# Optimization experiments

Measured on AMD Instinct MI355X. Metric: run time of the kernel, lower is better.

Reference implementation:

```python
import jax, jax.numpy as jnp
import numpy as np
import math

B, Hi, Wi, D = 4, 56, 56, 256
Ho, Wo = Hi // 2, Wi // 2
HEADS, HD = D // 32, 32
NUM_ITERS, DEPTH = 3, 2
KG, KB = 3, 7
LN_EPS = 1e-5

def _ln(x, g, b):
    m = x.mean(-1, keepdims=True)
    v = ((x - m) ** 2).mean(-1, keepdims=True)
    return (x - m) * jax.lax.rsqrt(v + LN_EPS) * g + b

def _na_idx(L, K):
    # NATten neighborhood: window clamped at borders, always K neighbors
    return jnp.clip(jnp.arange(L) - K // 2, 0, L - K)[:, None] + jnp.arange(K)[None, :]

def _gather_nb(t, K):  # t [B,n,H,W,D] -> [B,n,H,K,W,K,D]
    H, W = t.shape[2], t.shape[3]
    return t[:, :, _na_idx(H, K)][:, :, :, :, _na_idx(W, K)]

def _na2d_qk(query, key, K):  # query attends to K*K neighbors of key
    b, n, H, W, d = query.shape
    return jnp.einsum('bnijd,bniajcd->bnijac', query, _gather_nb(key, K)).reshape(b, n, H, W, K * K)

def _na2d_av(attn, v, K):
    b, n, H, W, _ = attn.shape
    return jnp.einsum('bnijac,bniajcd->bnijd', attn.reshape(b, n, H, W, K, K), _gather_nb(v, K))

def _rope_cos_sin(N, hd):
    f = 1.0 / (10000.0 ** (jnp.arange(0, hd, 2, dtype=jnp.float32) / hd))
    ang = jnp.arange(N, dtype=jnp.float32)[:, None] * f[None, :]
    return jnp.cos(ang), jnp.sin(ang)

def _apply_rope(x, cos, sin):  # x [B,N,h,hd], interleaved pairs
    x2 = x.reshape(x.shape[:-1] + (-1, 2))
    x0, x1 = x2[..., 0], x2[..., 1]
    c, s = cos[None, :, None, :], sin[None, :, None, :]
    return jnp.stack([x0 * c - x1 * s, x1 * c + x0 * s], -1).reshape(x.shape)

def _forward(x, g_seed_w, g_q_w, g_k_w, g_v_w, g_mlp_w1, g_mlp_b1, g_mlp_w2, g_mlp_b2,
             g_ln_in_g, g_ln_in_b, g_ln_out_g, g_ln_out_b, g_tau, g_rpb,
             blk_ln1_g, blk_ln1_b, blk_qkv_w, blk_proj_w, blk_proj_b,
             blk_ln2_g, blk_ln2_b, blk_mlp_w1, blk_mlp_b1, blk_mlp_w2, blk_mlp_b2):
    Bx = x.shape[0]
    ln_out = lambda t: _ln(t, g_ln_out_g, g_ln_out_b)

    def to_groups(t):  # [B,N_in,D] -> [B,4,Ho,Wo,D], group p = 2*ph+pw (F.unfold 2x2 s2 order)
        m = t.reshape(Bx, Ho, 2, Wo, 2, D).transpose(0, 2, 4, 1, 3, 5)
        return m.reshape(Bx, 4, Ho, Wo, D)

    # ---- SparseGroupingLayer (local) ----
    k = to_groups(_ln(x, g_ln_in_g, g_ln_in_b) @ g_k_w.T)
    v = to_groups(x @ g_v_w.T)
    seed = jax.lax.conv_general_dilated(
        x.reshape(Bx, Hi, Wi, D), g_seed_w.transpose(2, 3, 1, 0),
        (2, 2), ((1, 1), (1, 1)), dimension_numbers=('NHWC', 'HWIO', 'NHWC'))
    x_out = ln_out(seed.reshape(Bx, Ho * Wo, D))

    ih, iw = _na_idx(Ho, KG), _na_idx(Wo, KG)
    q_idx = (ih[:, None, :, None] * Wo + iw[None, :, None, :]).reshape(-1)  # [Ho*Wo*9]
    ids_full = jnp.tile(q_idx, 4)  # same idx map for all 4 groups
    rpb = g_rpb[None, :, None, None, :]
    scale_g = jnp.exp(g_tau[0])

    for _ in range(NUM_ITERS):
        q = (ln_out(x_out) @ g_q_w.T).reshape(Bx, 1, Ho, Wo, D)
        attn = _na2d_qk(k, jnp.broadcast_to(q, (Bx, 4, Ho, Wo, D)), KG) + rpb
        attn = jax.nn.softmax(attn * scale_g, axis=-1) + 1e-6  # [B,4,Ho,Wo,9]
        col = jnp.zeros((Bx, Ho * Wo), attn.dtype).at[:, ids_full].add(attn.reshape(Bx, -1))
        denom = col[:, ids_full].reshape(Bx, 4, Ho, Wo, KG * KG)
        A_col = attn / (denom + 1e-8)
        x_out = x_out + _na2d_av(A_col, v, KG).sum(axis=1).reshape(Bx, Ho * Wo, D)
        h = jax.nn.gelu(x_out @ g_mlp_w1.T + g_mlp_b1, approximate=False) @ g_mlp_w2.T + g_mlp_b2
        x_out = x_out + ln_out(h)

    # ---- SeNaTraBlocks (local neighborhood attention, window 7, RoPE) ----
    cos, sin = _rope_cos_sin(Ho * Wo, HD)
    sc = HD ** -0.5
    for l in range(DEPTH):
        h = _ln(x_out, blk_ln1_g[l], blk_ln1_b[l])
        qkv = (h @ blk_qkv_w[l].T).reshape(Bx, Ho * Wo, 3, HEADS, HD)
        q, kk, vv = qkv[:, :, 0], qkv[:, :, 1], qkv[:, :, 2]  # [B,N,h,hd]
        q = _apply_rope(q, cos, sin).transpose(0, 2, 1, 3).reshape(Bx, HEADS, Ho, Wo, HD)
        kk = _apply_rope(kk, cos, sin).transpose(0, 2, 1, 3).reshape(Bx, HEADS, Ho, Wo, HD)
        vv = vv.transpose(0, 2, 1, 3).reshape(Bx, HEADS, Ho, Wo, HD)
        a = jax.nn.softmax(_na2d_qk(q, kk, KB) * sc, axis=-1)
        o = _na2d_av(a, vv, KB).transpose(0, 2, 3, 1, 4).reshape(Bx, Ho * Wo, D)
        x_out = x_out + (o @ blk_proj_w[l].T + blk_proj_b[l])
        h2 = _ln(x_out, blk_ln2_g[l], blk_ln2_b[l])
        m = jax.nn.gelu(h2 @ blk_mlp_w1[l].T + blk_mlp_b1[l], approximate=False) @ blk_mlp_w2[l].T + blk_mlp_b2[l]
        x_out = x_out + m
    return x_out

def setup_inputs():
    key = jax.random.key(0)
    ks = jax.random.split(key, 16)
    w = lambda k, s: jax.random.normal(k, s, dtype=jnp.float32) * 0.02
    Hm = int(D * 3.0)
    return {
        'x': jax.random.normal(ks[0], (B, Hi * Wi, D), dtype=jnp.float32),
        'g_seed_w': w(ks[1], (D, D, 3, 3)),
        'g_q_w': w(ks[2], (D, D)), 'g_k_w': w(ks[3], (D, D)), 'g_v_w': w(ks[4], (D, D)),
        'g_mlp_w1': w(ks[5], (2 * D, D)), 'g_mlp_b1': jnp.zeros((2 * D,), jnp.float32),
        'g_mlp_w2': w(ks[6], (D, 2 * D)), 'g_mlp_b2': jnp.zeros((D,), jnp.float32),
        'g_ln_in_g': jnp.ones((D,), jnp.float32), 'g_ln_in_b': jnp.zeros((D,), jnp.float32),
        'g_ln_out_g': jnp.ones((D,), jnp.float32), 'g_ln_out_b': jnp.zeros((D,), jnp.float32),
        'g_tau': jnp.full((1,), math.log(D ** -0.5), jnp.float32),
        'g_rpb': w(ks[7], (4, 9)),
        'blk_ln1_g': jnp.ones((DEPTH, D), jnp.float32), 'blk_ln1_b': jnp.zeros((DEPTH, D), jnp.float32),
        'blk_qkv_w': w(ks[8], (DEPTH, 3 * D, D)),
        'blk_proj_w': w(ks[9], (DEPTH, D, D)), 'blk_proj_b': jnp.zeros((DEPTH, D), jnp.float32),
        'blk_ln2_g': jnp.ones((DEPTH, D), jnp.float32), 'blk_ln2_b': jnp.zeros((DEPTH, D), jnp.float32),
        'blk_mlp_w1': w(ks[10], (DEPTH, Hm, D)), 'blk_mlp_b1': jnp.zeros((DEPTH, Hm), jnp.float32),
        'blk_mlp_w2': w(ks[11], (DEPTH, D, Hm)), 'blk_mlp_b2': jnp.zeros((DEPTH, D), jnp.float32),
    }

def reference(x, g_seed_w, g_q_w, g_k_w, g_v_w, g_mlp_w1, g_mlp_b1, g_mlp_w2, g_mlp_b2,
              g_ln_in_g, g_ln_in_b, g_ln_out_g, g_ln_out_b, g_tau, g_rpb,
              blk_ln1_g, blk_ln1_b, blk_qkv_w, blk_proj_w, blk_proj_b,
              blk_ln2_g, blk_ln2_b, blk_mlp_w1, blk_mlp_b1, blk_mlp_w2, blk_mlp_b2):
    return _forward(x, g_seed_w, g_q_w, g_k_w, g_v_w, g_mlp_w1, g_mlp_b1, g_mlp_w2, g_mlp_b2,
                    g_ln_in_g, g_ln_in_b, g_ln_out_g, g_ln_out_b, g_tau, g_rpb,
                    blk_ln1_g, blk_ln1_b, blk_qkv_w, blk_proj_w, blk_proj_b,
                    blk_ln2_g, blk_ln2_b, blk_mlp_w1, blk_mlp_b1, blk_mlp_w2, blk_mlp_b2)
```

## Files before the change

kernel.cpp:

```cpp
#include <hip/hip_runtime.h>
#include <hip/hip_bf16.h>
#include <math.h>

typedef __hip_bfloat16 bf16;

#define LN_EPS 1e-5f

__device__ __forceinline__ float b2f(bf16 x){ return __bfloat162float(x); }
__device__ __forceinline__ float sanit(float s){ return fminf(fmaxf(s, -80.f), 80.f); }

__device__ __forceinline__ void stc(float* p, float v){ *p = v; }
__device__ __forceinline__ void stc(bf16* p, float v){ *p = __float2bfloat16(v); }

__device__ __forceinline__ short f2s(float f){
    union { __hip_bfloat16 h; short s; } u; u.h = __float2bfloat16(f); return u.s;
}
__device__ __forceinline__ float s2f(short s){
    union { short s; __hip_bfloat16 h; } u; u.s = s; return b2f(u.h);
}

using short8  = __attribute__((ext_vector_type(8))) short;
using floatx4 = __attribute__((ext_vector_type(4))) float;

__device__ __forceinline__ short8 load8(const float* p){
    float4 a1 = *(const float4*)p; float4 a2 = *(const float4*)(p+4);
    return (short8){ f2s(a1.x),f2s(a1.y),f2s(a1.z),f2s(a1.w),
                     f2s(a2.x),f2s(a2.y),f2s(a2.z),f2s(a2.w) };
}
__device__ __forceinline__ short8 load8(const bf16* p){ return *(const short8*)p; }

__global__ void setup_fused(const float* __restrict__ x, const float* __restrict__ g,
                            const float* __restrict__ bb, bf16* __restrict__ xln,
                            bf16* __restrict__ xh, float* __restrict__ tmpz,
                            const float* __restrict__ wq, const float* __restrict__ wk,
                            const float* __restrict__ wv, const float* __restrict__ m1,
                            const float* __restrict__ m2, const float* __restrict__ qkv,
                            const float* __restrict__ proj, const float* __restrict__ bm1,
                            const float* __restrict__ bm2, bf16* __restrict__ wdst,
                            const float* __restrict__ sw, bf16* __restrict__ swt)
{
    int blk = blockIdx.x; int tid = threadIdx.x;
    if (blk < 12544){
        int token = blk; int d = tid;
        int w = d >> 6, lane = d & 63;
        __shared__ float part[8];
        float v = x[(size_t)token*256 + d];
        float s = v;
        #pragma unroll
        for (int off=32; off>0; off>>=1) s += __shfl_down(s, off);
        if (lane==0) part[w] = s;
        __syncthreads();
        float mean = (part[0]+part[1]+part[2]+part[3]) * (1.f/256.f);
        float dev = v - mean;
        float q = dev*dev;
        __syncthreads();
        #pragma unroll
        for (int off=32; off>0; off>>=1) q += __shfl_down(q, off);
        if (lane==0) part[w+4] = q;
        __syncthreads();
        float var = (part[4]+part[5]+part[6]+part[7]) * (1.f/256.f);
        float r = dev*rsqrtf(var+LN_EPS)*g[d] + bb[d];
        size_t o = (size_t)token*256+d;
        xln[o] = __float2bfloat16(r);
        xh[o]  = __float2bfloat16(v);
        if (token < 3136) tmpz[(size_t)token*256 + d] = 0.f;
    } else if (blk < 19456){
        int i = (blk-12544)*256 + tid;
        const float* src; int off;
        if      (i <   65536){ src=wq;   off=i; }
        else if (i <  131072){ src=wk;   off=i-65536; }
        else if (i <  196608){ src=wv;   off=i-131072; }
        else if (i <  327680){ src=m1;   off=i-196608; }
        else if (i <  458752){ src=m2;   off=i-327680; }
        else if (i <  851968){ src=qkv;  off=i-458752; }
        else if (i <  983040){ src=proj; off=i-851968; }
        else if (i < 1376256){ src=bm1;  off=i-983040; }
        else                 { src=bm2;  off=i-1376256; }
        wdst[i] = __float2bfloat16(src[off]);
    } else {
        int idx = (blk-19456)*256 + tid;
        int o = idx/2304; int rem = idx - o*2304; int pos = rem>>8; int ci = rem&255;
        swt[idx] = __float2bfloat16(sw[(size_t)o*2304 + ci*9 + pos]);
    }
}

__global__ void ln_add_ln(const float* __restrict__ in, const float* __restrict__ resid,
                          const float* __restrict__ g1, const float* __restrict__ b1,
                          const float* __restrict__ g2, const float* __restrict__ b2,
                          float* __restrict__ xout, bf16* __restrict__ tmph,
                          float* __restrict__ colz)
{
    int token = blockIdx.x; int d = threadIdx.x;
    int w = d >> 6, lane = d & 63;
    __shared__ float part[8];
    size_t o = (size_t)token*256 + d;
    if (d == 0) colz[token] = 0.f;
    float v = in[o];
    float s = v;
    #pragma unroll
    for (int off=32; off>0; off>>=1) s += __shfl_down(s, off);
    if (lane==0) part[w] = s;
    __syncthreads();
    float mean = (part[0]+part[1]+part[2]+part[3]) * (1.f/256.f);
    float dev = v - mean;
    float q = dev*dev;
    __syncthreads();
    #pragma unroll
    for (int off=32; off>0; off>>=1) q += __shfl_down(q, off);
    if (lane==0) part[w+4] = q;
    __syncthreads();
    float var = (part[4]+part[5]+part[6]+part[7]) * (1.f/256.f);
    float r = dev*rsqrtf(var+LN_EPS)*g1[d] + b1[d];
    float sx = (resid ? resid[o] : 0.f) + r;
    xout[o] = sx;
    __syncthreads();
    float s2 = sx;
    #pragma unroll
    for (int off=32; off>0; off>>=1) s2 += __shfl_down(s2, off);
    if (lane==0) part[w] = s2;
    __syncthreads();
    float mean2 = (part[0]+part[1]+part[2]+part[3]) * (1.f/256.f);
    float dev2 = sx - mean2;
    float q2 = dev2*dev2;
    __syncthreads();
    #pragma unroll
    for (int off=32; off>0; off>>=1) q2 += __shfl_down(q2, off);
    if (lane==0) part[w+4] = q2;
    __syncthreads();
    float var2 = (part[4]+part[5]+part[6]+part[7]) * (1.f/256.f);
    tmph[o] = __float2bfloat16(dev2*rsqrtf(var2+LN_EPS)*g2[d] + b2[d]);
}

template<typename TO>
__global__ void ln256_kernel(const float* __restrict__ in, const float* __restrict__ g,
                             const float* __restrict__ bb, TO* __restrict__ out, int addTo)
{
    int token = blockIdx.x; int d = threadIdx.x;
    int w = d >> 6, lane = d & 63;
    __shared__ float part[8];
    float v = in[(size_t)token*256 + d];
    float s = v;
    #pragma unroll
    for (int off=32; off>0; off>>=1) s += __shfl_down(s, off);
    if (lane==0) part[w] = s;
    __syncthreads();
    float mean = (part[0]+part[1]+part[2]+part[3]) * (1.f/256.f);
    float dev = v - mean;
    float q = dev*dev;
    __syncthreads();
    #pragma unroll
    for (int off=32; off>0; off>>=1) q += __shfl_down(q, off);
    if (lane==0) part[w+4] = q;
    __syncthreads();
    float var = (part[4]+part[5]+part[6]+part[7]) * (1.f/256.f);
    float r = dev*rsqrtf(var+LN_EPS)*g[d] + bb[d];
    size_t o = (size_t)token*256+d;
    if (addTo) out[o] += r; else stc(&out[o], r);
}

template<typename TA, typename TC>
__global__ __launch_bounds__(128) void gemm_mfma(const TA* __restrict__ A,
                       const bf16* __restrict__ W,
                       const float* __restrict__ bias, const float* __restrict__ resid,
                       TC* __restrict__ C, int M, int N, int K, int do_gelu)
{
    __shared__ __align__(16) short As[2][32*40];
    __shared__ __align__(16) short Ws[2][64*40];
    int t = threadIdx.x;
    int n0 = blockIdx.x*64, m0 = blockIdx.y*32;
    int lane = t & 63, w = t >> 6;
    int quad = lane >> 4, mrow = lane & 15;
    floatx4 acc[4] = {{0,0,0,0},{0,0,0,0},{0,0,0,0},{0,0,0,0}};
    int r  = t >> 2;
    int kq = (t & 3) * 8;
    const TA*   Arow  = A + (size_t)(m0 + r)*K + kq;
    const bf16* Wrow0 = W + (size_t)(n0 + r)*K + kq;
    const bf16* Wrow1 = W + (size_t)(n0 + r + 32)*K + kq;

    short8 av  = load8(Arow);
    short8 wv0 = load8(Wrow0);
    short8 wv1 = load8(Wrow1);
    *(short8*)&As[0][r*40 + kq] = av;
    *(short8*)&Ws[0][r*40 + kq] = wv0;
    *(short8*)&Ws[0][(r+32)*40 + kq] = wv1;
    __syncthreads();

    int nb = K >> 5;
    int cur = 0;
    for (int i = 0; i < nb; i++){
        if (i+1 < nb){
            int k0 = (i+1) << 5;
            av  = load8(Arow + k0);
            wv0 = load8(Wrow0 + k0);
            wv1 = load8(Wrow1 + k0);
        }
        short8 af = *(short8*)&As[cur][(w*16 + mrow)*40 + quad*8];
        #pragma unroll
        for (int nt=0; nt<4; nt++){
            short8 bfv = *(short8*)&Ws[cur][(nt*16 + mrow)*40 + quad*8];
            acc[nt] = __builtin_amdgcn_mfma_f32_16x16x32_bf16(af, bfv, acc[nt], 0, 0, 0);
        }
        if (i+1 < nb){
            int nxt = cur ^ 1;
            *(short8*)&As[nxt][r*40 + kq] = av;
            *(short8*)&Ws[nxt][r*40 + kq] = wv0;
            *(short8*)&Ws[nxt][(r+32)*40 + kq] = wv1;
            __syncthreads();
            cur = nxt;
        }
    }
    #pragma unroll
    for (int nt=0; nt<4; nt++){
        int col = n0 + nt*16 + mrow;
        float bv = bias ? bias[col] : 0.f;
        #pragma unroll
        for (int rr=0; rr<4; rr++){
            int row = m0 + w*16 + quad*4 + rr;
            float v = acc[nt][rr] + bv;
            if (do_gelu) v = 0.5f*v*(1.0f+erff(v*0.70710678118654752f));
            size_t o = (size_t)row*N + col;
            if (resid) v += resid[o];
            stc(&C[o], v);
        }
    }
}

__global__ __launch_bounds__(128) void kv_conv(const bf16* __restrict__ xln,
                       const bf16* __restrict__ xh, const bf16* __restrict__ wk,
                       const bf16* __restrict__ wv, bf16* __restrict__ kp,
                       bf16* __restrict__ vp, const bf16* __restrict__ wt,
                       float* __restrict__ Cconv)
{
    __shared__ __align__(16) short As[2][32*40];
    __shared__ __align__(16) short Ws[2][64*40];
    int t = threadIdx.x;
    int lane = t & 63, w = t >> 6;
    int quad = lane >> 4, mrow = lane & 15;
    int r  = t >> 2;
    int kq = (t & 3) * 8;
    floatx4 acc[4] = {{0,0,0,0},{0,0,0,0},{0,0,0,0},{0,0,0,0}};
    int z = blockIdx.z;
    int n0 = blockIdx.x*64;

    if (z < 2){
        const int N = 256, K = 256;
        int m0 = blockIdx.y*32;
        const bf16* A = z ? xh : xln;
        const bf16* W = z ? wv : wk;
        bf16*       C = z ? vp : kp;
        const bf16* Arow  = A + (size_t)(m0 + r)*K + kq;
        const bf16* Wrow0 = W + (size_t)(n0 + r)*K + kq;
        const bf16* Wrow1 = W + (size_t)(n0 + r + 32)*K + kq;
        short8 av  = load8(Arow);
        short8 wv0 = load8(Wrow0);
        short8 wv1 = load8(Wrow1);
        *(short8*)&As[0][r*40 + kq] = av;
        *(short8*)&Ws[0][r*40 + kq] = wv0;
        *(short8*)&Ws[0][(r+32)*40 + kq] = wv1;
        __syncthreads();
        const int nb = K >> 5;
        int cur = 0;
        for (int i = 0; i < nb; i++){
            if (i+1 < nb){
                int k0 = (i+1) << 5;
                av  = load8(Arow + k0);
                wv0 = load8(Wrow0 + k0);
                wv1 = load8(Wrow1 + k0);
            }
            short8 af = *(short8*)&As[cur][(w*16 + mrow)*40 + quad*8];
            #pragma unroll
            for (int nt=0; nt<4; nt++){
                short8 bfv = *(short8*)&Ws[cur][(nt*16 + mrow)*40 + quad*8];
                acc[nt] = __builtin_amdgcn_mfma_f32_16x16x32_bf16(af, bfv, acc[nt], 0, 0, 0);
            }
            if (i+1 < nb){
                int nxt = cur ^ 1;
                *(short8*)&As[nxt][r*40 + kq] = av;
                *(short8*)&Ws[nxt][r*40 + kq] = wv0;
                *(short8*)&Ws[nxt][(r+32)*40 + kq] = wv1;
                __syncthreads();
                cur = nxt;
            }
        }
        #pragma unroll
        for (int nt=0; nt<4; nt++){
            int col = n0 + nt*16 + mrow;
            #pragma unroll
            for (int rr=0; rr<4; rr++){
                int row = m0 + w*16 + quad*4 + rr;
                C[(size_t)row*N + col] = __float2bfloat16(acc[nt][rr]);
            }
        }
    } else {
        int yy = blockIdx.y;
        if (yy >= 294) return;
        const int K = 2304, N = 256, KC = 768;
        int zc = yy / 98;
        int m0 = (yy - zc*98)*32;
        int m = m0 + r;
        int wo = m%28, ho = (m/28)%28, b = m/784;
        const bf16* Wrow0 = wt + (size_t)(n0 + r)*K + zc*KC + kq;
        const bf16* Wrow1 = wt + (size_t)(n0 + r + 32)*K + zc*KC + kq;
        int kh = zc;
        int ih = 2*ho + kh - 1;
        bool rowok = (ih>=0 && ih<56);
        auto loadA = [&](int k0)->short8{
            int kk = k0 + kq;
            int pos3 = kk >> 8;
            int ci = kk & 255;
            int iw = 2*wo + pos3 - 1;
            short8 a = {0,0,0,0,0,0,0,0};
            if (rowok && iw>=0 && iw<56)
                a = load8(xh + (((size_t)b*56 + ih)*56 + iw)*256 + ci);
            return a;
        };
        short8 av  = loadA(0);
        short8 wv0 = load8(Wrow0);
        short8 wv1 = load8(Wrow1);
        *(short8*)&As[0][r*40 + kq] = av;
        *(short8*)&Ws[0][r*40 + kq] = wv0;
        *(short8*)&Ws[0][(r+32)*40 + kq] = wv1;
        __syncthreads();
        const int nb = KC >> 5;
        int cur = 0;
        for (int i = 0; i < nb; i++){
            if (i+1 < nb){
                int k0 = (i+1) << 5;
                av  = loadA(k0);
                wv0 = load8(Wrow0 + k0);
                wv1 = load8(Wrow1 + k0);
            }
            short8 af = *(short8*)&As[cur][(w*16 + mrow)*40 + quad*8];
            #pragma unroll
            for (int nt=0; nt<4; nt++){
                short8 bfv = *(short8*)&Ws[cur][(nt*16 + mrow)*40 + quad*8];
                acc[nt] = __builtin_amdgcn_mfma_f32_16x16x32_bf16(af, bfv, acc[nt], 0, 0, 0);
            }
            if (i+1 < nb){
                int nxt = cur ^ 1;
                *(short8*)&As[nxt][r*40 + kq] = av;
                *(short8*)&Ws[nxt][r*40 + kq] = wv0;
                *(short8*)&Ws[nxt][(r+32)*40 + kq] = wv1;
                __syncthreads();
                cur = nxt;
            }
        }
        #pragma unroll
        for (int nt=0; nt<4; nt++){
            int col = n0 + nt*16 + mrow;
            #pragma unroll
            for (int rr=0; rr<4; rr++){
                int row = m0 + w*16 + quad*4 + rr;
                atomicAdd(&Cconv[(size_t)row*N + col], acc[nt][rr]);
            }
        }
    }
}

__global__ __launch_bounds__(256) void grp_attn_row(const bf16* __restrict__ kproj,
                                const bf16* __restrict__ qbuf,
                                const float* __restrict__ rpb, const float* __restrict__ g_tau,
                                float* __restrict__ attn, float* __restrict__ col)
{
    int blk = blockIdx.x;
    int i = blk % 28; int bn = blk / 28; int n = bn & 3; int b = bn >> 2;
    int tid = threadIdx.x;
    int sh = n>>1, sw = n&1;
    int i0 = min(max(i-1,0),25);
    __shared__ short Ks[28*256];
    __shared__ short Qs[3*28*256];
    __shared__ float sc[28*9];
    __shared__ float pr[28*9];

    for (int u = tid; u < 28*32; u += 256){
        int j = u >> 5, c = u & 31;
        *(short8*)&Ks[j*256 + c*8] =
            *(const short8*)(kproj + ((size_t)b*3136 + (2*i+sh)*56 + (2*j+sw))*256 + c*8);
    }
    for (int u = tid; u < 3*28*32; u += 256){
        int r = u / (28*32); int rem = u - r*(28*32);
        int j = rem >> 5, c = rem & 31;
        *(short8*)&Qs[(r*28 + j)*256 + c*8] =
            *(const short8*)(qbuf + ((size_t)b*784 + (i0+r)*28 + j)*256 + c*8);
    }
    __syncthreads();

    float scale = expf(g_tau[0]);
    if (tid < 252){
        int pix = tid / 9, l = tid - (tid/9)*9;
        int j0 = min(max(pix-1,0),25);
        int qr = l/3, qj = j0 + (l - qr*3);
        const short* kp = &Ks[pix*256];
        const short* qp = &Qs[(qr*28 + qj)*256];
        float p = 0.f;
        for (int c = 0; c < 32; c++){
            short8 k8 = *(const short8*)(kp + c*8);
            short8 q8 = *(const short8*)(qp + c*8);
            #pragma unroll
            for (int d=0; d<8; d++) p += s2f(k8[d])*s2f(q8[d]);
        }
        sc[pix*9 + l] = sanit((p + rpb[n*9+l])*scale);
    }
    __syncthreads();
    if (tid < 28){
        float m = -1e30f;
        for (int l=0;l<9;l++) m = fmaxf(m, sc[tid*9+l]);
        float sum=0.f; float e[9];
        for (int l=0;l<9;l++){ e[l]=expf(sc[tid*9+l]-m); sum+=e[l]; }
        float inv = 1.f/fmaxf(sum,1e-30f);
        for (int l=0;l<9;l++) pr[tid*9+l] = e[l]*inv + 1e-6f;
    }
    __syncthreads();
    if (tid < 252){
        int pix = tid/9, l = tid - (tid/9)*9;
        float a = pr[pix*9+l];
        int idx = (b*4+n)*784 + i*28 + pix;
        attn[(size_t)idx*9 + l] = a;
        int j0 = min(max(pix-1,0),25);
        int qi = i0 + l/3, qj = j0 + l%3;
        atomicAdd(&col[b*784 + qi*28 + qj], a);
    }
}

__global__ void grp_av_kernel(const float* __restrict__ attn, const float* __restrict__ col,
                              const bf16* __restrict__ vproj, float* __restrict__ xout,
                              bf16* __restrict__ xouth)
{
    int idx = blockIdx.x;
    int j = idx%28; int i = (idx/28)%28; int b = idx/784;
    int d = threadIdx.x;
    int i0 = min(max(i-1,0),25), j0 = min(max(j-1,0),25);
    float acc = 0.f;
    for (int n=0; n<4; n++){
        int sh = n>>1, sw = n&1;
        const float* ap = attn + ((size_t)(b*4+n)*784 + i*28+j)*9;
        for (int l=0; l<9; l++){
            int qi = i0 + l/3, qj = j0 + l%3;
            float dv = col[b*784 + qi*28+qj] + 1e-8f;
            acc += (ap[l]/dv) * b2f(vproj[((size_t)b*3136 + (2*qi+sh)*56 + (2*qj+sw))*256 + d]);
        }
    }
    size_t o = (size_t)idx*256 + d;
    float nv = xout[o] + acc;
    xout[o] = nv;
    xouth[o] = __float2bfloat16(nv);
}

__global__ __launch_bounds__(256) void blk_attn_row(const bf16* __restrict__ qkv,
                                                    bf16* __restrict__ obuf)
{
    int blk = blockIdx.x;
    int h = blk & 7; int rest = blk >> 3;
    int i = rest % 28; int b = rest / 28;
    int tid = threadIdx.x;
    int i0 = min(max(i-3,0),21);

    __shared__ float Ks[7*28*32];
    __shared__ float Vs[7*28*32];
    __shared__ float Qs[28*32];
    __shared__ float Ps[28*52];

    const float LOG1E4_16 = 0.5756462732485115f;

    for (int idx = tid; idx < 196*4; idx += 256){
        int pos = idx >> 2, u8 = idx & 3;
        int ki = i0 + pos/28, kj = pos - (pos/28)*28;
        int ttok = ki*28 + kj;
        const bf16* base = qkv + ((size_t)(b*784 + ttok))*768 + h*32 + u8*8;
        short8 k8 = *(const short8*)(base + 256);
        short8 v8 = *(const short8*)(base + 512);
        float f[8];
        #pragma unroll
        for (int d=0; d<8; d++) f[d] = s2f(k8[d]);
        #pragma unroll
        for (int m2=0; m2<4; m2++){
            int u = u8*4 + m2;
            float ang = (float)ttok * expf(-(float)u * LOG1E4_16);
            float c = cosf(ang), s = sinf(ang);
            float x0 = f[2*m2], x1 = f[2*m2+1];
            f[2*m2]   = x0*c - x1*s;
            f[2*m2+1] = x1*c + x0*s;
        }
        #pragma unroll
        for (int d=0; d<8; d++){
            Ks[pos*32 + u8*8 + d] = f[d];
            Vs[pos*32 + u8*8 + d] = s2f(v8[d]);
        }
    }
    for (int idx = tid; idx < 28*4; idx += 256){
        int tt = idx >> 2, u8 = idx & 3;
        int ttok = i*28 + tt;
        const bf16* base = qkv + ((size_t)(b*784 + ttok))*768 + h*32 + u8*8;
        short8 q8 = *(const short8*)base;
        float f[8];
        #pragma unroll
        for (int d=0; d<8; d++) f[d] = s2f(q8[d]);
        #pragma unroll
        for (int m2=0; m2<4; m2++){
            int u = u8*4 + m2;
            float ang = (float)ttok * expf(-(float)u * LOG1E4_16);
            float c = cosf(ang), s = sinf(ang);
            float x0 = f[2*m2], x1 = f[2*m2+1];
            f[2*m2]   = x0*c - x1*s;
            f[2*m2+1] = x1*c + x0*s;
        }
        #pragma unroll
        for (int d=0; d<8; d++) Qs[tt*32 + u8*8 + d] = f[d];
    }
    __syncthreads();

    int tt = tid >> 3, s = tid & 7;
    float sc[7];
    float mx = -1e30f;
    int j0 = min(max(tt-3,0),21);
    if (tt < 28){
        int c = 0;
        for (int l = s; l < 49; l += 8, c++){
            int ki = l/7, kj = j0 + l - (l/7)*7;
            const float4* kp = (const float4*)&Ks[(ki*28+kj)*32];
            const float4* qp = (const float4*)&Qs[tt*32];
            float p = 0.f;
            #pragma unroll
            for (int d=0; d<8; d++){
                float4 kv4 = kp[d], qv4 = qp[d];
                p += qv4.x*kv4.x + qv4.y*kv4.y + qv4.z*kv4.z + qv4.w*kv4.w;
            }
            sc[c] = sanit(p * 0.17677669529663687f);
            mx = fmaxf(mx, sc[c]);
        }
    }
    #pragma unroll
    for (int off=1; off<8; off<<=1) mx = fmaxf(mx, __shfl_xor(mx, off, 8));
    float sm = 0.f;
    if (tt < 28){
        int c = 0;
        for (int l = s; l < 49; l += 8, c++){ sc[c] = expf(sc[c]-mx); sm += sc[c]; }
    }
    #pragma unroll
    for (int off=1; off<8; off<<=1) sm += __shfl_xor(sm, off, 8);
    if (tt < 28){
        float inv = 1.f/fmaxf(sm, 1e-30f);
        int c = 0;
        for (int l = s; l < 49; l += 8, c++) Ps[tt*52 + l] = sc[c]*inv;
    }
    __syncthreads();

    for (int o = tid; o < 28*32; o += 256){
        int t2 = o >> 5, d = o & 31;
        int jj0 = min(max(t2-3,0),21);
        float acc = 0.f;
        #pragma unroll 7
        for (int l=0; l<49; l++){
            int ki = l/7, kj = jj0 + l - (l/7)*7;
            acc += Ps[t2*52 + l] * Vs[(ki*28+kj)*32 + d];
        }
        obuf[((size_t)(b*784 + i*28 + t2))*256 + h*32 + d] = __float2bfloat16(acc);
    }
}

extern "C" void kernel_launch(void* const* d_in, const int* in_sizes, int n_in,
                              void* d_out, int out_size, void* d_ws, size_t ws_size,
                              hipStream_t stream) {
    const float* x         = (const float*)d_in[0];
    const float* g_seed_w  = (const float*)d_in[1];
    const float* g_q_w     = (const float*)d_in[2];
    const float* g_k_w     = (const float*)d_in[3];
    const float* g_v_w     = (const float*)d_in[4];
    const float* g_mlp_w1  = (const float*)d_in[5];
    const float* g_mlp_b1  = (const float*)d_in[6];
    const float* g_mlp_w2  = (const float*)d_in[7];
    const float* g_mlp_b2  = (const float*)d_in[8];
    const float* g_ln_in_g = (const float*)d_in[9];
    const float* g_ln_in_b = (const float*)d_in[10];
    const float* g_ln_out_g= (const float*)d_in[11];
    const float* g_ln_out_b= (const float*)d_in[12];
    const float* g_tau     = (const float*)d_in[13];
    const float* g_rpb     = (const float*)d_in[14];
    const float* blk_ln1_g = (const float*)d_in[15];
    const float* blk_ln1_b = (const float*)d_in[16];
    const float* blk_qkv_w = (const float*)d_in[17];
    const float* blk_proj_w= (const float*)d_in[18];
    const float* blk_proj_b= (const float*)d_in[19];
    const float* blk_ln2_g = (const float*)d_in[20];
    const float* blk_ln2_b = (const float*)d_in[21];
    const float* blk_mlp_w1= (const float*)d_in[22];
    const float* blk_mlp_b1= (const float*)d_in[23];
    const float* blk_mlp_w2= (const float*)d_in[24];
    const float* blk_mlp_b2= (const float*)d_in[25];

    float* f      = (float*)d_ws;
    bf16*  wbuf   = (bf16*)d_ws;
    bf16*  kproj  = (bf16*)(f + 1179648);
    bf16*  vproj  = (bf16*)(f + 2785280);
    float* xout   = f + 4390912;
    float* tmp    = f + 5193728;
    bf16*  tmph   = (bf16*)(f + 5996544);
    bf16*  qbufh  = (bf16*)(f + 6397952);
    bf16*  bigh   = (bf16*)(f + 6799360);
    float* attng  = f + 8003584;
    float* col    = f + 8116480;
    bf16*  xln    = (bf16*)(f + 8119616);
    bf16*  xh     = (bf16*)(f + 9725248);
    bf16*  xouth  = (bf16*)(f + 11330880);

    bf16* w_q    = wbuf;
    bf16* w_k    = wbuf + 65536;
    bf16* w_v    = wbuf + 131072;
    bf16* w_m1   = wbuf + 196608;
    bf16* w_m2   = wbuf + 327680;
    bf16* w_qkv  = wbuf + 458752;
    bf16* w_proj = wbuf + 851968;
    bf16* w_bm1  = wbuf + 983040;
    bf16* w_bm2  = wbuf + 1376256;
    bf16* w_seed = wbuf + 1769472;

    setup_fused<<<21760, 256, 0, stream>>>(x, g_ln_in_g, g_ln_in_b, xln, xh, tmp,
                                           g_q_w, g_k_w, g_v_w, g_mlp_w1, g_mlp_w2,
                                           blk_qkv_w, blk_proj_w, blk_mlp_w1, blk_mlp_w2,
                                           wbuf, g_seed_w, w_seed);
    kv_conv<<<dim3(4,392,3), 128, 0, stream>>>(xln, xh, w_k, w_v, kproj, vproj, w_seed, tmp);
    ln_add_ln<<<3136, 256, 0, stream>>>(tmp, nullptr, g_ln_out_g, g_ln_out_b,
                                        g_ln_out_g, g_ln_out_b, xout, tmph, col);

    for (int it=0; it<3; it++){
        gemm_mfma<bf16,bf16><<<dim3(4,98), 128, 0, stream>>>(tmph, w_q, nullptr, nullptr, qbufh, 3136,256,256, 0);
        grp_attn_row<<<448, 256, 0, stream>>>(kproj, qbufh, g_rpb, g_tau, attng, col);
        grp_av_kernel<<<3136, 256, 0, stream>>>(attng, col, vproj, xout, xouth);
        gemm_mfma<bf16,bf16><<<dim3(8,98), 128, 0, stream>>>(xouth, w_m1, g_mlp_b1, nullptr, bigh, 3136,512,256, 1);
        gemm_mfma<bf16,float><<<dim3(4,98), 128, 0, stream>>>(bigh, w_m2, g_mlp_b2, nullptr, tmp, 3136,256,512, 0);
        const float* g2 = (it<2) ? g_ln_out_g : blk_ln1_g;
        const float* b2 = (it<2) ? g_ln_out_b : blk_ln1_b;
        ln_add_ln<<<3136, 256, 0, stream>>>(tmp, xout, g_ln_out_g, g_ln_out_b,
                                            g2, b2, xout, tmph, col);
    }

    for (int l=0; l<2; l++){
        gemm_mfma<bf16,bf16><<<dim3(12,98), 128, 0, stream>>>(tmph, w_qkv + (size_t)l*196608, nullptr, nullptr, bigh, 3136,768,256, 0);
        blk_attn_row<<<896, 256, 0, stream>>>(bigh, qbufh);
        gemm_mfma<bf16,float><<<dim3(4,98), 128, 0, stream>>>(qbufh, w_proj + (size_t)l*65536, blk_proj_b + l*256, xout, xout, 3136,256,256, 0);
        ln256_kernel<bf16><<<3136, 256, 0, stream>>>(xout, blk_ln2_g + l*256, blk_ln2_b + l*256, tmph, 0);
        gemm_mfma<bf16,bf16><<<dim3(12,98), 128, 0, stream>>>(tmph, w_bm1 + (size_t)l*196608, blk_mlp_b1 + l*768, nullptr, bigh, 3136,768,256, 1);
        if (l==0){
            gemm_mfma<bf16,float><<<dim3(4,98), 128, 0, stream>>>(bigh, w_bm2, blk_mlp_b2, xout, xout, 3136,256,768, 0);
            ln256_kernel<bf16><<<3136, 256, 0, stream>>>(xout, blk_ln1_g + 256, blk_ln1_b + 256, tmph, 0);
        } else {
            gemm_mfma<bf16,float><<<dim3(4,98), 128, 0, stream>>>(bigh, w_bm2 + 196608, blk_mlp_b2 + 256, xout, (float*)d_out, 3136,256,768, 0);
        }
    }
}
```

Baseline: 503.0 us.

## Fuse grouping iterations into one cooperative persistent kernel with grid syncs

New measurement: 1.734 ms. 245% more time.

```diff
diff --git a/kernel.cpp b/kernel.cpp
--- a/kernel.cpp
+++ b/kernel.cpp
@@ -1,7 +1,9 @@
 #include <hip/hip_runtime.h>
+#include <hip/hip_cooperative_groups.h>
 #include <hip/hip_bf16.h>
 #include <math.h>
 
+namespace cg = cooperative_groups;
 typedef __hip_bfloat16 bf16;
 
 #define LN_EPS 1e-5f
@@ -82,53 +84,6 @@
         int o = idx/2304; int rem = idx - o*2304; int pos = rem>>8; int ci = rem&255;
         swt[idx] = __float2bfloat16(sw[(size_t)o*2304 + ci*9 + pos]);
     }
-}
-
-__global__ void ln_add_ln(const float* __restrict__ in, const float* __restrict__ resid,
-                          const float* __restrict__ g1, const float* __restrict__ b1,
-                          const float* __restrict__ g2, const float* __restrict__ b2,
-                          float* __restrict__ xout, bf16* __restrict__ tmph,
-                          float* __restrict__ colz)
-{
-    int token = blockIdx.x; int d = threadIdx.x;
-    int w = d >> 6, lane = d & 63;
-    __shared__ float part[8];
-    size_t o = (size_t)token*256 + d;
-    if (d == 0) colz[token] = 0.f;
-    float v = in[o];
-    float s = v;
-    #pragma unroll
-    for (int off=32; off>0; off>>=1) s += __shfl_down(s, off);
-    if (lane==0) part[w] = s;
-    __syncthreads();
-    float mean = (part[0]+part[1]+part[2]+part[3]) * (1.f/256.f);
-    float dev = v - mean;
-    float q = dev*dev;
-    __syncthreads();
-    #pragma unroll
-    for (int off=32; off>0; off>>=1) q += __shfl_down(q, off);
-    if (lane==0) part[w+4] = q;
-    __syncthreads();
-    float var = (part[4]+part[5]+part[6]+part[7]) * (1.f/256.f);
-    float r = dev*rsqrtf(var+LN_EPS)*g1[d] + b1[d];
-    float sx = (resid ? resid[o] : 0.f) + r;
-    xout[o] = sx;
-    __syncthreads();
-    float s2 = sx;
-    #pragma unroll
-    for (int off=32; off>0; off>>=1) s2 += __shfl_down(s2, off);
-    if (lane==0) part[w] = s2;
-    __syncthreads();
-    float mean2 = (part[0]+part[1]+part[2]+part[3]) * (1.f/256.f);
-    float dev2 = sx - mean2;
-    float q2 = dev2*dev2;
-    __syncthreads();
-    #pragma unroll
-    for (int off=32; off>0; off>>=1) q2 += __shfl_down(q2, off);
-    if (lane==0) part[w+4] = q2;
-    __syncthreads();
-    float var2 = (part[4]+part[5]+part[6]+part[7]) * (1.f/256.f);
-    tmph[o] = __float2bfloat16(dev2*rsqrtf(var2+LN_EPS)*g2[d] + b2[d]);
 }
 
 template<typename TO>
@@ -357,93 +312,230 @@
     }
 }
 
-__global__ __launch_bounds__(256) void grp_attn_row(const bf16* __restrict__ kproj,
-                                const bf16* __restrict__ qbuf,
-                                const float* __restrict__ rpb, const float* __restrict__ g_tau,
-                                float* __restrict__ attn, float* __restrict__ col)
-{
-    int blk = blockIdx.x;
-    int i = blk % 28; int bn = blk / 28; int n = bn & 3; int b = bn >> 2;
+struct MegaP {
+    const bf16 *kproj, *vproj, *w_q, *w_m1, *w_m2;
+    bf16 *tmph, *qbufh, *bigh, *xouth;
+    float *tmp, *xout, *attng, *col;
+    const float *lnog, *lnob, *blk1g, *blk1b, *b_m1, *b_m2, *rpb, *g_tau;
+};
+
+__device__ void gemm_stage(const bf16* A, const bf16* W, const float* bias,
+                           bf16* Cb, float* Cf, int M, int N, int K, int do_gelu,
+                           char* smem)
+{
+    short* As = (short*)smem;
+    short* Ws = As + 5120;
+    int t = threadIdx.x;
+    int lane = t & 63, w = t >> 6;
+    int quad = lane >> 4, mrow = lane & 15;
+    int r = t >> 2, kq = (t & 3)*8;
+    int ntN = N >> 6;
+    int ntot = (M >> 6) * ntN;
+    for (int tile = blockIdx.x; tile < ntot; tile += gridDim.x){
+        int m0 = (tile / ntN) << 6, n0 = (tile % ntN) << 6;
+        floatx4 acc[4] = {{0,0,0,0},{0,0,0,0},{0,0,0,0},{0,0,0,0}};
+        const bf16* Arow = A + (size_t)(m0 + r)*K + kq;
+        const bf16* Wrow = W + (size_t)(n0 + r)*K + kq;
+        short8 av = load8(Arow);
+        short8 wv = load8(Wrow);
+        __syncthreads();
+        *(short8*)&As[r*40 + kq] = av;
+        *(short8*)&Ws[r*40 + kq] = wv;
+        __syncthreads();
+        int nb = K >> 5, cur = 0;
+        for (int i = 0; i < nb; i++){
+            if (i+1 < nb){
+                int k0 = (i+1) << 5;
+                av = load8(Arow + k0);
+                wv = load8(Wrow + k0);
+            }
+            short8 af = *(short8*)&As[cur*2560 + (w*16+mrow)*40 + quad*8];
+            #pragma unroll
+            for (int nt=0; nt<4; nt++){
+                short8 bfv = *(short8*)&Ws[cur*2560 + (nt*16+mrow)*40 + quad*8];
+                acc[nt] = __builtin_amdgcn_mfma_f32_16x16x32_bf16(af, bfv, acc[nt], 0,0,0);
+            }
+            if (i+1 < nb){
+                int nxt = cur ^ 1;
+                *(short8*)&As[nxt*2560 + r*40 + kq] = av;
+                *(short8*)&Ws[nxt*2560 + r*40 + kq] = wv;
+                __syncthreads();
+                cur = nxt;
+            }
+        }
+        #pragma unroll
+        for (int nt=0; nt<4; nt++){
+            int col = n0 + nt*16 + mrow;
+            float bv = bias ? bias[col] : 0.f;
+            #pragma unroll
+            for (int rr=0; rr<4; rr++){
+                int row = m0 + w*16 + quad*4 + rr;
+                float v = acc[nt][rr] + bv;
+                if (do_gelu) v = 0.5f*v*(1.0f+erff(v*0.70710678118654752f));
+                size_t o = (size_t)row*N + col;
+                if (Cf) Cf[o] = v; else Cb[o] = __float2bfloat16(v);
+            }
+        }
+    }
+}
+
+__device__ void lnaddln_stage(const float* in, const float* resid, const float* g1,
+                              const float* b1, const float* g2, const float* b2,
+                              float* xout, bf16* tmph, float* colz, char* smem)
+{
+    float* part = (float*)smem;
+    int d = threadIdx.x;
+    int w = d >> 6, lane = d & 63;
+    for (int token = blockIdx.x; token < 3136; token += gridDim.x){
+        __syncthreads();
+        size_t o = (size_t)token*256 + d;
+        if (d == 0) colz[token] = 0.f;
+        float v = in[o];
+        float s = v;
+        #pragma unroll
+        for (int off=32; off>0; off>>=1) s += __shfl_down(s, off);
+        if (lane==0) part[w] = s;
+        __syncthreads();
+        float mean = (part[0]+part[1]+part[2]+part[3]) * (1.f/256.f);
+        float dev = v - mean;
+        float q = dev*dev;
+        __syncthreads();
+        #pragma unroll
+        for (int off=32; off>0; off>>=1) q += __shfl_down(q, off);
+        if (lane==0) part[w+4] = q;
+        __syncthreads();
+        float var = (part[4]+part[5]+part[6]+part[7]) * (1.f/256.f);
+        float r = dev*rsqrtf(var+LN_EPS)*g1[d] + b1[d];
+        float sx = (resid ? resid[o] : 0.f) + r;
+        xout[o] = sx;
+        __syncthreads();
+        float s2 = sx;
+        #pragma unroll
+        for (int off=32; off>0; off>>=1) s2 += __shfl_down(s2, off);
+        if (lane==0) part[w] = s2;
+        __syncthreads();
+        float mean2 = (part[0]+part[1]+part[2]+part[3]) * (1.f/256.f);
+        float dev2 = sx - mean2;
+        float q2 = dev2*dev2;
+        __syncthreads();
+        #pragma unroll
+        for (int off=32; off>0; off>>=1) q2 += __shfl_down(q2, off);
+        if (lane==0) part[w+4] = q2;
+        __syncthreads();
+        float var2 = (part[4]+part[5]+part[6]+part[7]) * (1.f/256.f);
+        tmph[o] = __float2bfloat16(dev2*rsqrtf(var2+LN_EPS)*g2[d] + b2[d]);
+    }
+}
+
+__device__ void grpattn_stage(const bf16* kproj, const bf16* qbuf, const float* rpb,
+                              const float* g_tau, float* attn, float* col, char* smem)
+{
+    short* Ks = (short*)smem;
+    short* Qs = Ks + 7168;
+    float* sc = (float*)(smem + 57344);
+    float* pr = sc + 252;
     int tid = threadIdx.x;
-    int sh = n>>1, sw = n&1;
-    int i0 = min(max(i-1,0),25);
-    __shared__ short Ks[28*256];
-    __shared__ short Qs[3*28*256];
-    __shared__ float sc[28*9];
-    __shared__ float pr[28*9];
-
-    for (int u = tid; u < 28*32; u += 256){
-        int j = u >> 5, c = u & 31;
-        *(short8*)&Ks[j*256 + c*8] =
-            *(const short8*)(kproj + ((size_t)b*3136 + (2*i+sh)*56 + (2*j+sw))*256 + c*8);
-    }
-    for (int u = tid; u < 3*28*32; u += 256){
-        int r = u / (28*32); int rem = u - r*(28*32);
-        int j = rem >> 5, c = rem & 31;
-        *(short8*)&Qs[(r*28 + j)*256 + c*8] =
-            *(const short8*)(qbuf + ((size_t)b*784 + (i0+r)*28 + j)*256 + c*8);
-    }
-    __syncthreads();
-
-    float scale = expf(g_tau[0]);
-    if (tid < 252){
-        int pix = tid / 9, l = tid - (tid/9)*9;
-        int j0 = min(max(pix-1,0),25);
-        int qr = l/3, qj = j0 + (l - qr*3);
-        const short* kp = &Ks[pix*256];
-        const short* qp = &Qs[(qr*28 + qj)*256];
-        float p = 0.f;
-        for (int c = 0; c < 32; c++){
-            short8 k8 = *(const short8*)(kp + c*8);
-            short8 q8 = *(const short8*)(qp + c*8);
-            #pragma unroll
-            for (int d=0; d<8; d++) p += s2f(k8[d])*s2f(q8[d]);
-        }
-        sc[pix*9 + l] = sanit((p + rpb[n*9+l])*scale);
-    }
-    __syncthreads();
-    if (tid < 28){
-        float m = -1e30f;
-        for (int l=0;l<9;l++) m = fmaxf(m, sc[tid*9+l]);
-        float sum=0.f; float e[9];
-        for (int l=0;l<9;l++){ e[l]=expf(sc[tid*9+l]-m); sum+=e[l]; }
-        float inv = 1.f/fmaxf(sum,1e-30f);
-        for (int l=0;l<9;l++) pr[tid*9+l] = e[l]*inv + 1e-6f;
-    }
-    __syncthreads();
-    if (tid < 252){
-        int pix = tid/9, l = tid - (tid/9)*9;
-        float a = pr[pix*9+l];
-        int idx = (b*4+n)*784 + i*28 + pix;
-        attn[(size_t)idx*9 + l] = a;
-        int j0 = min(max(pix-1,0),25);
-        int qi = i0 + l/3, qj = j0 + l%3;
-        atomicAdd(&col[b*784 + qi*28 + qj], a);
-    }
-}
-
-__global__ void grp_av_kernel(const float* __restrict__ attn, const float* __restrict__ col,
-                              const bf16* __restrict__ vproj, float* __restrict__ xout,
-                              bf16* __restrict__ xouth)
-{
-    int idx = blockIdx.x;
-    int j = idx%28; int i = (idx/28)%28; int b = idx/784;
+    for (int blk = blockIdx.x; blk < 448; blk += gridDim.x){
+        __syncthreads();
+        int i = blk % 28; int bn = blk / 28; int n = bn & 3; int b = bn >> 2;
+        int sh = n>>1, sw = n&1;
+        int i0 = min(max(i-1,0),25);
+        for (int u = tid; u < 28*32; u += 256){
+            int j = u >> 5, c = u & 31;
+            *(short8*)&Ks[j*256 + c*8] =
+                *(const short8*)(kproj + ((size_t)b*3136 + (2*i+sh)*56 + (2*j+sw))*256 + c*8);
+        }
+        for (int u = tid; u < 3*28*32; u += 256){
+            int rr = u / (28*32); int rem = u - rr*(28*32);
+            int j = rem >> 5, c = rem & 31;
+            *(short8*)&Qs[(rr*28 + j)*256 + c*8] =
+                *(const short8*)(qbuf + ((size_t)b*784 + (i0+rr)*28 + j)*256 + c*8);
+        }
+        __syncthreads();
+        float scale = expf(g_tau[0]);
+        if (tid < 252){
+            int pix = tid / 9, l = tid - (tid/9)*9;
+            int j0 = min(max(pix-1,0),25);
+            int qr = l/3, qj = j0 + (l - qr*3);
+            const short* kp = &Ks[pix*256];
+            const short* qp = &Qs[(qr*28 + qj)*256];
+            float p = 0.f;
+            for (int c = 0; c < 32; c++){
+                short8 k8 = *(const short8*)(kp + c*8);
+                short8 q8 = *(const short8*)(qp + c*8);
+                #pragma unroll
+                for (int d=0; d<8; d++) p += s2f(k8[d])*s2f(q8[d]);
+            }
+            sc[pix*9 + l] = sanit((p + rpb[n*9+l])*scale);
+        }
+        __syncthreads();
+        if (tid < 28){
+            float m = -1e30f;
+            for (int l=0;l<9;l++) m = fmaxf(m, sc[tid*9+l]);
+            float sum=0.f; float e[9];
+            for (int l=0;l<9;l++){ e[l]=expf(sc[tid*9+l]-m); sum+=e[l]; }
+            float inv = 1.f/fmaxf(sum,1e-30f);
+            for (int l=0;l<9;l++) pr[tid*9+l] = e[l]*inv + 1e-6f;
+        }
+        __syncthreads();
+        if (tid < 252){
+            int pix = tid/9, l = tid - (tid/9)*9;
+            float a = pr[pix*9+l];
+            int idx = (b*4+n)*784 + i*28 + pix;
+            attn[(size_t)idx*9 + l] = a;
+            int j0 = min(max(pix-1,0),25);
+            int qi = i0 + l/3, qj = j0 + l%3;
+            atomicAdd(&col[b*784 + qi*28 + qj], a);
+        }
+    }
+}
+
+__device__ void grpav_stage(const float* attn, const float* col, const bf16* vproj,
+                            float* xout, bf16* xouth)
+{
     int d = threadIdx.x;
-    int i0 = min(max(i-1,0),25), j0 = min(max(j-1,0),25);
-    float acc = 0.f;
-    for (int n=0; n<4; n++){
-        int sh = n>>1, sw = n&1;
-        const float* ap = attn + ((size_t)(b*4+n)*784 + i*28+j)*9;
-        for (int l=0; l<9; l++){
-            int qi = i0 + l/3, qj = j0 + l%3;
-            float dv = col[b*784 + qi*28+qj] + 1e-8f;
-            acc += (ap[l]/dv) * b2f(vproj[((size_t)b*3136 + (2*qi+sh)*56 + (2*qj+sw))*256 + d]);
-        }
-    }
-    size_t o = (size_t)idx*256 + d;
-    float nv = xout[o] + acc;
-    xout[o] = nv;
-    xouth[o] = __float2bfloat16(nv);
+    for (int idx = blockIdx.x; idx < 3136; idx += gridDim.x){
+        int j = idx%28; int i = (idx/28)%28; int b = idx/784;
+        int i0 = min(max(i-1,0),25), j0 = min(max(j-1,0),25);
+        float acc = 0.f;
+        for (int n=0; n<4; n++){
+            int sh = n>>1, sw = n&1;
+            const float* ap = attn + ((size_t)(b*4+n)*784 + i*28+j)*9;
+            for (int l=0; l<9; l++){
+                int qi = i0 + l/3, qj = j0 + l%3;
+                float dv = col[b*784 + qi*28+qj] + 1e-8f;
+                acc += (ap[l]/dv) * b2f(vproj[((size_t)b*3136 + (2*qi+sh)*56 + (2*qj+sw))*256 + d]);
+            }
+        }
+        size_t o = (size_t)idx*256 + d;
+        float nv = xout[o] + acc;
+        xout[o] = nv;
+        xouth[o] = __float2bfloat16(nv);
+    }
+}
+
+__global__ __launch_bounds__(256, 2) void mega_iter(MegaP p)
+{
+    cg::grid_group grid = cg::this_grid();
+    __shared__ __align__(16) char smem[59392];
+    lnaddln_stage(p.tmp, nullptr, p.lnog, p.lnob, p.lnog, p.lnob, p.xout, p.tmph, p.col, smem);
+    grid.sync();
+    for (int it = 0; it < 3; it++){
+        gemm_stage(p.tmph, p.w_q, nullptr, p.qbufh, nullptr, 3136, 256, 256, 0, smem);
+        grid.sync();
+        grpattn_stage(p.kproj, p.qbufh, p.rpb, p.g_tau, p.attng, p.col, smem);
+        grid.sync();
+        grpav_stage(p.attng, p.col, p.vproj, p.xout, p.xouth);
+        grid.sync();
+        gemm_stage(p.xouth, p.w_m1, p.b_m1, p.bigh, nullptr, 3136, 512, 256, 1, smem);
+        grid.sync();
+        gemm_stage(p.bigh, p.w_m2, p.b_m2, nullptr, p.tmp, 3136, 256, 512, 0, smem);
+        grid.sync();
+        const float* g2 = (it < 2) ? p.lnog : p.blk1g;
+        const float* b2 = (it < 2) ? p.lnob : p.blk1b;
+        lnaddln_stage(p.tmp, p.xout, p.lnog, p.lnob, g2, b2, p.xout, p.tmph, p.col, smem);
+        grid.sync();
+    }
 }
 
 __global__ __launch_bounds__(256) void blk_attn_row(const bf16* __restrict__ qkv,
@@ -619,20 +711,19 @@
                                            blk_qkv_w, blk_proj_w, blk_mlp_w1, blk_mlp_w2,
                                            wbuf, g_seed_w, w_seed);
     kv_conv<<<dim3(4,392,3), 128, 0, stream>>>(xln, xh, w_k, w_v, kproj, vproj, w_seed, tmp);
-    ln_add_ln<<<3136, 256, 0, stream>>>(tmp, nullptr, g_ln_out_g, g_ln_out_b,
-                                        g_ln_out_g, g_ln_out_b, xout, tmph, col);
-
-    for (int it=0; it<3; it++){
-        gemm_mfma<bf16,bf16><<<dim3(4,98), 128, 0, stream>>>(tmph, w_q, nullptr, nullptr, qbufh, 3136,256,256, 0);
-        grp_attn_row<<<448, 256, 0, stream>>>(kproj, qbufh, g_rpb, g_tau, attng, col);
-        grp_av_kernel<<<3136, 256, 0, stream>>>(attng, col, vproj, xout, xouth);
-        gemm_mfma<bf16,bf16><<<dim3(8,98), 128, 0, stream>>>(xouth, w_m1, g_mlp_b1, nullptr, bigh, 3136,512,256, 1);
-        gemm_mfma<bf16,float><<<dim3(4,98), 128, 0, stream>>>(bigh, w_m2, g_mlp_b2, nullptr, tmp, 3136,256,512, 0);
-        const float* g2 = (it<2) ? g_ln_out_g : blk_ln1_g;
-        const float* b2 = (it<2) ? g_ln_out_b : blk_ln1_b;
-        ln_add_ln<<<3136, 256, 0, stream>>>(tmp, xout, g_ln_out_g, g_ln_out_b,
-                                            g2, b2, xout, tmph, col);
-    }
+
+    MegaP p;
+    p.kproj = kproj; p.vproj = vproj; p.w_q = w_q; p.w_m1 = w_m1; p.w_m2 = w_m2;
+    p.tmph = tmph; p.qbufh = qbufh; p.bigh = bigh; p.xouth = xouth;
+    p.tmp = tmp; p.xout = xout; p.attng = attng; p.col = col;
+    p.lnog = g_ln_out_g; p.lnob = g_ln_out_b; p.blk1g = blk_ln1_g; p.blk1b = blk_ln1_b;
+    p.b_m1 = g_mlp_b1; p.b_m2 = g_mlp_b2; p.rpb = g_rpb; p.g_tau = g_tau;
+    int bpc = 0;
+    hipOccupancyMaxActiveBlocksPerMultiprocessor(&bpc, mega_iter, 256, 0);
+    if (bpc < 1) bpc = 1;
+    int grid = bpc * 256; if (grid > 512) grid = 512;
+    void* args[] = { (void*)&p };
+    hipLaunchCooperativeKernel((void*)mega_iter, dim3(grid), dim3(256), args, 0, stream);
 
     for (int l=0; l<2; l++){
         gemm_mfma<bf16,bf16><<<dim3(12,98), 128, 0, stream>>>(tmph, w_qkv + (size_t)l*196608, nullptr, nullptr, bigh, 3136,768,256, 0);
```

## Fuse grouping-layer MLP GEMMs into one kernel with hidden activations in LDS

Applied to the files above, without the earlier changes.

New measurement: 608.5 us. 21.0% more time.

```diff
diff --git a/kernel.cpp b/kernel.cpp
--- a/kernel.cpp
+++ b/kernel.cpp
@@ -221,6 +221,114 @@
             size_t o = (size_t)row*N + col;
             if (resid) v += resid[o];
             stc(&C[o], v);
+        }
+    }
+}
+
+__global__ __launch_bounds__(128) void fused_mlp(const bf16* __restrict__ X,
+        const bf16* __restrict__ W1, const float* __restrict__ b1,
+        const bf16* __restrict__ W2, const float* __restrict__ b2,
+        float* __restrict__ Out)
+{
+    __shared__ __align__(16) short Xs[32*264];
+    __shared__ __align__(16) short Hs[32*520];
+    __shared__ __align__(16) short Ws[2][64*40];
+    int t = threadIdx.x;
+    int m0 = blockIdx.x*32;
+    int lane = t & 63, w = t >> 6;
+    int quad = lane >> 4, mrow = lane & 15;
+    int r = t >> 2, kq = (t & 3)*8;
+
+    #pragma unroll
+    for (int c = 0; c < 8; c++)
+        *(short8*)&Xs[r*264 + c*32 + kq] = load8(X + (size_t)(m0+r)*256 + c*32 + kq);
+
+    for (int ht = 0; ht < 8; ht++){
+        floatx4 acc[4] = {{0,0,0,0},{0,0,0,0},{0,0,0,0},{0,0,0,0}};
+        const bf16* W1r0 = W1 + (size_t)(ht*64 + r)*256 + kq;
+        const bf16* W1r1 = W1 + (size_t)(ht*64 + r + 32)*256 + kq;
+        short8 wv0 = load8(W1r0);
+        short8 wv1 = load8(W1r1);
+        __syncthreads();
+        *(short8*)&Ws[0][r*40+kq] = wv0;
+        *(short8*)&Ws[0][(r+32)*40+kq] = wv1;
+        __syncthreads();
+        int cur = 0;
+        for (int i = 0; i < 8; i++){
+            if (i+1 < 8){
+                int k0 = (i+1) << 5;
+                wv0 = load8(W1r0 + k0);
+                wv1 = load8(W1r1 + k0);
+            }
+            short8 af = *(short8*)&Xs[(w*16+mrow)*264 + i*32 + quad*8];
+            #pragma unroll
+            for (int nt=0; nt<4; nt++){
+                short8 bfv = *(short8*)&Ws[cur][(nt*16+mrow)*40 + quad*8];
+                acc[nt] = __builtin_amdgcn_mfma_f32_16x16x32_bf16(af, bfv, acc[nt], 0,0,0);
+            }
+            if (i+1 < 8){
+                int nxt = cur ^ 1;
+                *(short8*)&Ws[nxt][r*40+kq] = wv0;
+                *(short8*)&Ws[nxt][(r+32)*40+kq] = wv1;
+                __syncthreads();
+                cur = nxt;
+            }
+        }
+        #pragma unroll
+        for (int nt=0; nt<4; nt++){
+            int col = ht*64 + nt*16 + mrow;
+            float bv = b1[col];
+            #pragma unroll
+            for (int rr=0; rr<4; rr++){
+                int row = w*16 + quad*4 + rr;
+                float v = acc[nt][rr] + bv;
+                v = 0.5f*v*(1.0f+erff(v*0.70710678118654752f));
+                Hs[row*520 + col] = f2s(v);
+            }
+        }
+    }
+    __syncthreads();
+
+    for (int nt2 = 0; nt2 < 4; nt2++){
+        floatx4 acc[4] = {{0,0,0,0},{0,0,0,0},{0,0,0,0},{0,0,0,0}};
+        const bf16* W2r0 = W2 + (size_t)(nt2*64 + r)*512 + kq;
+        const bf16* W2r1 = W2 + (size_t)(nt2*64 + r + 32)*512 + kq;
+        short8 wv0 = load8(W2r0);
+        short8 wv1 = load8(W2r1);
+        __syncthreads();
+        *(short8*)&Ws[0][r*40+kq] = wv0;
+        *(short8*)&Ws[0][(r+32)*40+kq] = wv1;
+        __syncthreads();
+        int cur = 0;
+        for (int i = 0; i < 16; i++){
+            if (i+1 < 16){
+                int k0 = (i+1) << 5;
+                wv0 = load8(W2r0 + k0);
+                wv1 = load8(W2r1 + k0);
+            }
+            short8 af = *(short8*)&Hs[(w*16+mrow)*520 + i*32 + quad*8];
+            #pragma unroll
+            for (int nt=0; nt<4; nt++){
+                short8 bfv = *(short8*)&Ws[cur][(nt*16+mrow)*40 + quad*8];
+                acc[nt] = __builtin_amdgcn_mfma_f32_16x16x32_bf16(af, bfv, acc[nt], 0,0,0);
+            }
+            if (i+1 < 16){
+                int nxt = cur ^ 1;
+                *(short8*)&Ws[nxt][r*40+kq] = wv0;
+                *(short8*)&Ws[nxt][(r+32)*40+kq] = wv1;
+                __syncthreads();
+                cur = nxt;
+            }
+        }
+        #pragma unroll
+        for (int nt=0; nt<4; nt++){
+            int col = nt2*64 + nt*16 + mrow;
+            float bv = b2[col];
+            #pragma unroll
+            for (int rr=0; rr<4; rr++){
+                int row = m0 + w*16 + quad*4 + rr;
+                Out[(size_t)row*256 + col] = acc[nt][rr] + bv;
+            }
         }
     }
 }
@@ -626,8 +734,7 @@
         gemm_mfma<bf16,bf16><<<dim3(4,98), 128, 0, stream>>>(tmph, w_q, nullptr, nullptr, qbufh, 3136,256,256, 0);
         grp_attn_row<<<448, 256, 0, stream>>>(kproj, qbufh, g_rpb, g_tau, attng, col);
         grp_av_kernel<<<3136, 256, 0, stream>>>(attng, col, vproj, xout, xouth);
-        gemm_mfma<bf16,bf16><<<dim3(8,98), 128, 0, stream>>>(xouth, w_m1, g_mlp_b1, nullptr, bigh, 3136,512,256, 1);
-        gemm_mfma<bf16,float><<<dim3(4,98), 128, 0, stream>>>(bigh, w_m2, g_mlp_b2, nullptr, tmp, 3136,256,512, 0);
+        fused_mlp<<<98, 128, 0, stream>>>(xouth, w_m1, g_mlp_b1, w_m2, g_mlp_b2, tmp);
         const float* g2 = (it<2) ? g_ln_out_g : blk_ln1_g;
         const float* b2 = (it<2) ? g_ln_out_b : blk_ln1_b;
         ln_add_ln<<<3136, 256, 0, stream>>>(tmp, xout, g_ln_out_g, g_ln_out_b,
```
